# Kernel optimization log

Measured on AMD Instinct MI355X. Metric: run time of the kernel, lower is better.

Reference implementation:

```python
import jax, jax.numpy as jnp
import numpy as np

B, N, C = 32, 262144, 5
ALPHA = 50.0
EPS_LS = 0.2
BASE_W = [0.8, 2.0, 1.5, 1.5, 3.5]
# (cid, ref, sign): height_diff = sign*(pr_z[cid] - gt_z[ref]); violation = sigmoid(-10*diff)
# Enumerates all z_above / z_below pairs in the hierarchy dict.
PAIRS = [(1, 2, -1.0), (1, 3, -1.0), (1, 4, -1.0),
         (2, 1, 1.0), (2, 3, -1.0), (2, 4, -1.0),
         (3, 1, 1.0), (3, 2, 1.0), (3, 4, -1.0),
         (4, 1, 1.0), (4, 2, 1.0), (4, 3, 1.0)]


def setup_inputs() -> dict:
    key = jax.random.key(0)
    k1, k2, k3 = jax.random.split(key, 3)
    outputs = jax.random.normal(k1, (B, C, N), dtype=jnp.float32)
    labels = jax.random.randint(k2, (B, N), 0, C, dtype=jnp.int32)
    points = jax.random.normal(k3, (B, N, 3), dtype=jnp.float32)
    return {"outputs": outputs, "labels": labels, "points": points}


def _centroid(points, mask):
    # points: [B,N,3], mask: [B,N] bool -> ([B,3], [B] valid)
    valid = mask.any(axis=1)
    m = mask.astype(points.dtype)
    s = jnp.einsum('bn,bnd->bd', m, points)
    cnt = jnp.clip(m.sum(axis=1), 1.0)
    return s / cnt[:, None], valid


def _forward(outputs, points, labels):
    logits = jnp.transpose(outputs, (0, 2, 1))  # [B,N,C]
    b = labels.shape[0]
    preds = jnp.argmax(logits, axis=-1)  # [B,N]
    base = jnp.asarray(BASE_W, dtype=logits.dtype)
    weights = jnp.broadcast_to(base, (b, C))
    gt_c = {cid: _centroid(points, labels == cid) for cid in (1, 2, 3, 4)}
    pr_c = {cid: _centroid(points, preds == cid) for cid in (1, 2, 3, 4)}
    # hierarchy violation scatter into per-batch class weights
    for cid, ref, sign in PAIRS:
        pr_pos, pos_valid = pr_c[cid]
        gt_ref, ref_valid = gt_c[ref]
        valid = ref_valid & pos_valid
        diff = sign * (pr_pos[:, 2] - gt_ref[:, 2])
        add = jnp.where(valid, ALPHA * jax.nn.sigmoid(-diff * 10.0), 0.0)
        weights = weights.at[:, cid].add(add).at[:, ref].add(0.3 * add)
    # predicted bounding boxes of masked points (zeros included, as in torch)
    bounds = {}
    for cid in (2, 3):
        mp = points * (preds == cid)[:, :, None].astype(points.dtype)
        bounds[cid] = jnp.stack([mp.min(axis=1), mp.max(axis=1)], axis=1)  # [B,2,3]
    for cid in (2, 3):
        rb = bounds[3 if cid == 2 else 2]
        xc = (bounds[cid][:, :, 0] - rb[:, 0:1, 0]) / (rb[:, 1:2, 0] - rb[:, 0:1, 0] + 1e-7)
        yc = (bounds[cid][:, :, 1] - rb[:, 0:1, 1]) / (rb[:, 1:2, 1] - rb[:, 0:1, 1] + 1e-7)
        viol = ((xc < 0.1) | (xc > 0.9)) | ((yc < 0.1) | (yc > 0.9))
        weights = weights.at[:, cid].add(ALPHA * viol.astype(weights.dtype).mean(axis=1))
    weights = jnp.clip(weights, 0.1, 10.0)
    # inverse-sqrt class frequency weights
    dist = jnp.bincount(labels.reshape(-1), length=C).astype(logits.dtype)
    cw = 1.0 / (jnp.sqrt(dist) + 1e-7)
    cw = cw / cw.sum() * C
    w = weights.mean(axis=0) * cw  # [C]
    # weighted cross entropy with label_smoothing=0.2 (PyTorch semantics)
    logp = jax.nn.log_softmax(logits.reshape(-1, C), axis=-1)
    y = labels.reshape(-1)
    wt = w[y]
    wsum = wt.sum()
    nll = (wt * -jnp.take_along_axis(logp, y[:, None], axis=1)[:, 0]).sum() / wsum
    smooth = (-(logp * w[None, :]).sum(axis=-1)).sum() / wsum
    return (1.0 - EPS_LS) * nll + (EPS_LS / C) * smooth


def reference(outputs, labels, points):
    return _forward(outputs, points, labels)
```

## Files before the change

### kernel.cpp

```cpp
#include <hip/hip_runtime.h>
#include <math.h>

#define NPTS 262144
#define BATCH 32

__device__ __forceinline__ float wred_sum(float v) {
#pragma unroll
    for (int o = 32; o; o >>= 1) v += __shfl_down(v, o);
    return v;
}
__device__ __forceinline__ unsigned wred_usum(unsigned v) {
#pragma unroll
    for (int o = 32; o; o >>= 1) v += __shfl_down(v, o);
    return v;
}


__global__ __launch_bounds__(256) void bsl_main(
    const float* __restrict__ outputs, const int* __restrict__ labels,
    const float* __restrict__ points, float* __restrict__ pf,
    unsigned int* __restrict__ pi, int bpb, int iters,
    unsigned int* __restrict__ counter)
{
    const int blk = blockIdx.x;
    const int nblk = gridDim.x;
    const int b = blk / bpb;
    const int seg = blk % bpb;
    const int seg_start = seg * (iters * 1024);
    const int tid = threadIdx.x;

    if (blk == 0 && tid == 0) *counter = 0u;

    float S[5] = {0, 0, 0, 0, 0};
    float T[5] = {0, 0, 0, 0, 0};
    float lseacc = 0.f;
    float gtz[4] = {0, 0, 0, 0};
    float prz[4] = {0, 0, 0, 0};
    const float INF = __int_as_float(0x7f800000);
    float mn2x = INF, mx2x = -INF, mn2y = INF, mx2y = -INF;
    float mn3x = INF, mx3x = -INF, mn3y = INF, mx3y = -INF;
    unsigned bc[5] = {0, 0, 0, 0, 0}, prc[4] = {0, 0, 0, 0};

    const float* obase = outputs + (size_t)b * 5 * NPTS;
    const int*   lbase = labels + (size_t)b * NPTS;
    const float* pbase = points + (size_t)b * NPTS * 3;

    for (int it = 0; it < iters; ++it) {
        const int n = seg_start + it * 1024 + tid * 4;
        float4 L[5];
#pragma unroll
        for (int c = 0; c < 5; ++c)
            L[c] = *(const float4*)(obase + (size_t)c * NPTS + n);
        const int4 lab = *(const int4*)(lbase + n);
        const float4* pp = (const float4*)(pbase + (size_t)n * 3);
        const float4 p0 = pp[0], p1 = pp[1], p2 = pp[2];
        const float xs[4] = {p0.x, p0.w, p1.z, p2.y};
        const float ys[4] = {p0.y, p1.x, p1.w, p2.z};
        const float zs[4] = {p0.z, p1.y, p2.x, p2.w};
        const int   lb[4] = {lab.x, lab.y, lab.z, lab.w};
#pragma unroll
        for (int j = 0; j < 4; ++j) {
            float v[5];
#pragma unroll
            for (int c = 0; c < 5; ++c) v[c] = ((const float*)&L[c])[j];
            float best = v[0]; int pred = 0;
#pragma unroll
            for (int c = 1; c < 5; ++c)
                if (v[c] > best) { best = v[c]; pred = c; }
            float e = 0.f;
#pragma unroll
            for (int c = 0; c < 5; ++c) e += __expf(v[c] - best);
            const float lse = best + __logf(e);
            lseacc += lse;
            const int y = lb[j];
#pragma unroll
            for (int c = 0; c < 5; ++c) {
                S[c] += v[c];
                const bool is = (y == c);
                T[c] += is ? (lse - v[c]) : 0.f;
                bc[c] += is ? 1u : 0u;
            }
            const float z = zs[j];
#pragma unroll
            for (int k = 0; k < 4; ++k) {
                const bool gy = (y == k + 1), py = (pred == k + 1);
                gtz[k] += gy ? z : 0.f;
                prz[k] += py ? z : 0.f;
                prc[k] += py ? 1u : 0u;
            }
            const float x = xs[j], yv = ys[j];
            const float a2x = (pred == 2) ? x : 0.f;
            const float a2y = (pred == 2) ? yv : 0.f;
            const float a3x = (pred == 3) ? x : 0.f;
            const float a3y = (pred == 3) ? yv : 0.f;
            mn2x = fminf(mn2x, a2x); mx2x = fmaxf(mx2x, a2x);
            mn2y = fminf(mn2y, a2y); mx2y = fmaxf(mx2y, a2y);
            mn3x = fminf(mn3x, a3x); mx3x = fmaxf(mx3x, a3x);
            mn3y = fminf(mn3y, a3y); mx3y = fmaxf(mx3y, a3y);
        }
    }

    float fv[27] = {S[0], S[1], S[2], S[3], S[4],
                    T[0], T[1], T[2], T[3], T[4],
                    lseacc,
                    gtz[0], gtz[1], gtz[2], gtz[3],
                    prz[0], prz[1], prz[2], prz[3],
                    mn2x, mx2x, mn2y, mx2y, mn3x, mx3x, mn3y, mx3y};
    unsigned iv[9] = {bc[0], bc[1], bc[2], bc[3], bc[4],
                      prc[0], prc[1], prc[2], prc[3]};

    __shared__ float sf[4][27];
    __shared__ unsigned si[4][9];
    const int wid = tid >> 6, lane = tid & 63;
#pragma unroll
    for (int vdx = 0; vdx < 27; ++vdx) {
        float r;
        if (vdx < 19) r = wred_sum(fv[vdx]);
        else if (((vdx - 19) & 1) == 0) {
#pragma unroll
            for (int o = 32; o; o >>= 1) fv[vdx] = fminf(fv[vdx], __shfl_down(fv[vdx], o));
            r = fv[vdx];
        } else {
#pragma unroll
            for (int o = 32; o; o >>= 1) fv[vdx] = fmaxf(fv[vdx], __shfl_down(fv[vdx], o));
            r = fv[vdx];
        }
        if (lane == 0) sf[wid][vdx] = r;
    }
#pragma unroll
    for (int vdx = 0; vdx < 9; ++vdx) {
        unsigned r = wred_usum(iv[vdx]);
        if (lane == 0) si[wid][vdx] = r;
    }
    __syncthreads();
    if (tid == 0) {
#pragma unroll
        for (int vdx = 0; vdx < 27; ++vdx) {
            float r;
            if (vdx < 19) r = sf[0][vdx] + sf[1][vdx] + sf[2][vdx] + sf[3][vdx];
            else if (((vdx - 19) & 1) == 0)
                r = fminf(fminf(sf[0][vdx], sf[1][vdx]), fminf(sf[2][vdx], sf[3][vdx]));
            else
                r = fmaxf(fmaxf(sf[0][vdx], sf[1][vdx]), fmaxf(sf[2][vdx], sf[3][vdx]));
            pf[(size_t)vdx * nblk + blk] = r;
        }
#pragma unroll
        for (int vdx = 0; vdx < 9; ++vdx)
            pi[(size_t)vdx * nblk + blk] = si[0][vdx] + si[1][vdx] + si[2][vdx] + si[3][vdx];
    }
}

__global__ __launch_bounds__(256) void bsl_tail(
    const float* __restrict__ pf, const unsigned int* __restrict__ pi,
    int bpb, float* __restrict__ s2, unsigned int* __restrict__ counter,
    float* __restrict__ out)
{
    const int nblk = BATCH * bpb;
    const int t = blockIdx.x;
    const int tid = threadIdx.x;
    const int wid = tid >> 6, lane = tid & 63;
    __shared__ float red[4];
    __shared__ int isLast;
    __shared__ float sm[16 + 24 * BATCH];

    if (t < 16) {
        float s;
        if (t < 11) {
            const float4* p4 = (const float4*)(pf + (size_t)t * nblk);
            const float4 a = p4[tid], b = p4[tid + 256];
            s = ((a.x + a.y) + (a.z + a.w)) + ((b.x + b.y) + (b.z + b.w));
        } else {
            const uint4* p4 = (const uint4*)(pi + (size_t)(t - 11) * nblk);
            const uint4 a = p4[tid], b = p4[tid + 256];
            s = ((float)a.x + (float)a.y + (float)a.z + (float)a.w) +
                ((float)b.x + (float)b.y + (float)b.z + (float)b.w);
        }
        s = wred_sum(s);
        if (lane == 0) red[wid] = s;
        __syncthreads();
        if (tid == 0) s2[t] = red[0] + red[1] + red[2] + red[3];
    } else {
        const int b = tid >> 3;
        const int k = tid & 7;
        const int base = b * bpb;
        const int f = t - 16;
        float r;
        if (f < 8) {
            const float4* p4 = (const float4*)(pf + (size_t)(11 + f) * nblk + base);
            const float4 a = p4[k], c = p4[k + 8];
            r = ((a.x + a.y) + (a.z + a.w)) + ((c.x + c.y) + (c.z + c.w));
#pragma unroll
            for (int o = 4; o; o >>= 1) r += __shfl_xor(r, o);
        } else if (f < 16) {
            const int g = f - 8;
            const bool ismin = ((g & 1) == 0);
            const float4* p4 = (const float4*)(pf + (size_t)(19 + g) * nblk + base);
            const float4 a = p4[k], c = p4[k + 8];
            if (ismin) {
                r = fminf(fminf(fminf(a.x, a.y), fminf(a.z, a.w)),
                          fminf(fminf(c.x, c.y), fminf(c.z, c.w)));
#pragma unroll
                for (int o = 4; o; o >>= 1) r = fminf(r, __shfl_xor(r, o));
            } else {
                r = fmaxf(fmaxf(fmaxf(a.x, a.y), fmaxf(a.z, a.w)),
                          fmaxf(fmaxf(c.x, c.y), fmaxf(c.z, c.w)));
#pragma unroll
                for (int o = 4; o; o >>= 1) r = fmaxf(r, __shfl_xor(r, o));
            }
        } else {
            const int g = f - 16;
            const int row = (g < 4) ? (1 + g) : (5 + (g - 4));
            const uint4* p4 = (const uint4*)(pi + (size_t)row * nblk + base);
            const uint4 a = p4[k], c = p4[k + 8];
            r = ((float)a.x + (float)a.y + (float)a.z + (float)a.w) +
                ((float)c.x + (float)c.y + (float)c.z + (float)c.w);
#pragma unroll
            for (int o = 4; o; o >>= 1) r += __shfl_xor(r, o);
        }
        if (k == 0) s2[16 + b * 24 + ((f < 8) ? f : (f < 16) ? (8 + f - 8) : (16 + f - 16))] = r;
        __syncthreads();
    }

    if (tid == 0) {
        __threadfence();
        const unsigned old = atomicAdd(counter, 1u);
        isLast = (old == (unsigned)(gridDim.x - 1)) ? 1 : 0;
    }
    __syncthreads();
    if (!isLast) return;
    __threadfence();

    for (int i = tid; i < 16 + 24 * BATCH; i += 256) sm[i] = s2[i];
    __syncthreads();
    if (wid != 0) return;

    const float BASE_W[5] = {0.8f, 2.0f, 1.5f, 1.5f, 3.5f};
    const int pc[12]  = {1, 1, 1, 2, 2, 2, 3, 3, 3, 4, 4, 4};
    const int prf[12] = {2, 3, 4, 1, 3, 4, 1, 2, 4, 1, 2, 3};
    const float ps[12] = {-1.f, -1.f, -1.f, 1.f, -1.f, -1.f, 1.f, 1.f, -1.f, 1.f, 1.f, 1.f};

    float w[5] = {0, 0, 0, 0, 0};
    if (lane < BATCH) {
        const float* R = sm + 16 + lane * 24;
        for (int c = 0; c < 5; ++c) w[c] = BASE_W[c];
        float gtm[4], prm[4];
        bool gv[4], pv[4];
#pragma unroll
        for (int k = 0; k < 4; ++k) {
            const float c1 = R[16 + k];
            gv[k] = (c1 > 0.f);
            gtm[k] = R[k] / fmaxf(c1, 1.f);
            const float c2 = R[20 + k];
            pv[k] = (c2 > 0.f);
            prm[k] = R[4 + k] / fmaxf(c2, 1.f);
        }
#pragma unroll
        for (int p = 0; p < 12; ++p) {
            const int cid = pc[p], ref = prf[p];
            float add = 0.f;
            if (pv[cid - 1] && gv[ref - 1]) {
                const float diff = ps[p] * (prm[cid - 1] - gtm[ref - 1]);
                add = 50.f / (1.f + expf(10.f * diff));
            }
            w[cid] += add;
            w[ref] += 0.3f * add;
        }
        const float mn2x = R[8],  mx2x = R[9],  mn2y = R[10], mx2y = R[11];
        const float mn3x = R[12], mx3x = R[13], mn3y = R[14], mx3y = R[15];
        {
            const float dx = mx3x - mn3x + 1e-7f, dy = mx3y - mn3y + 1e-7f;
            const float xc0 = (mn2x - mn3x) / dx, xc1 = (mx2x - mn3x) / dx;
            const float yc0 = (mn2y - mn3y) / dy, yc1 = (mx2y - mn3y) / dy;
            const float v0 = (xc0 < 0.1f || xc0 > 0.9f || yc0 < 0.1f || yc0 > 0.9f) ? 1.f : 0.f;
            const float v1 = (xc1 < 0.1f || xc1 > 0.9f || yc1 < 0.1f || yc1 > 0.9f) ? 1.f : 0.f;
            w[2] += 50.f * 0.5f * (v0 + v1);
        }
        {
            const float dx = mx2x - mn2x + 1e-7f, dy = mx2y - mn2y + 1e-7f;
            const float xc0 = (mn3x - mn2x) / dx, xc1 = (mx3x - mn2x) / dx;
            const float yc0 = (mn3y - mn2y) / dy, yc1 = (mx3y - mn2y) / dy;
            const float v0 = (xc0 < 0.1f || xc0 > 0.9f || yc0 < 0.1f || yc0 > 0.9f) ? 1.f : 0.f;
            const float v1 = (xc1 < 0.1f || xc1 > 0.9f || yc1 < 0.1f || yc1 > 0.9f) ? 1.f : 0.f;
            w[3] += 50.f * 0.5f * (v0 + v1);
        }
#pragma unroll
        for (int c = 0; c < 5; ++c)
            w[c] = fminf(fmaxf(w[c], 0.1f), 10.f);
    }
    float wsumc[5];
#pragma unroll
    for (int c = 0; c < 5; ++c) wsumc[c] = wred_sum(w[c]);

    if (lane == 0) {
        float dist[5], cw[5], s = 0.f;
#pragma unroll
        for (int c = 0; c < 5; ++c) {
            dist[c] = sm[11 + c];
            cw[c] = 1.f / (sqrtf(dist[c]) + 1e-7f);
            s += cw[c];
        }
        float wf[5], wsum = 0.f, W = 0.f, nllnum = 0.f, Ssum = 0.f;
#pragma unroll
        for (int c = 0; c < 5; ++c) {
            cw[c] = cw[c] / s * 5.f;
            wf[c] = (wsumc[c] / 32.f) * cw[c];
            wsum += wf[c] * dist[c];
            W += wf[c];
            nllnum += wf[c] * sm[5 + c];
            Ssum += wf[c] * sm[c];
        }
        const float nll = nllnum / wsum;
        const float smooth = (W * sm[10] - Ssum) / wsum;
        out[0] = 0.8f * nll + 0.04f * smooth;
    }
}

extern "C" void kernel_launch(void* const* d_in, const int* in_sizes, int n_in,
                              void* d_out, int out_size, void* d_ws, size_t ws_size,
                              hipStream_t stream) {
    const float* outputs = (const float*)d_in[0];
    const int*   labels  = (const int*)d_in[1];
    const float* points  = (const float*)d_in[2];
    float* out = (float*)d_out;

    const size_t S2N = 16 + 24 * BATCH;
    const int bpb = 64;
    const int nblk = BATCH * bpb;
    const int iters = NPTS / (bpb * 1024);

    float* pf = (float*)d_ws;
    unsigned int* pi = (unsigned int*)(pf + (size_t)27 * nblk);
    float* s2 = (float*)(pi + (size_t)9 * nblk);
    unsigned int* counter = (unsigned int*)(s2 + S2N);

    bsl_main<<<nblk, 256, 0, stream>>>(outputs, labels, points, pf, pi, bpb, iters, counter);
    bsl_tail<<<40, 256, 0, stream>>>(pf, pi, bpb, s2, counter, out);
}
```

Before: 68.24 us.

## Fuse main and tail kernels using atomic counter handoff to last blocks

```diff
diff --git a/kernel.cpp b/kernel.cpp
--- a/kernel.cpp
+++ b/kernel.cpp
@@ -3,6 +3,11 @@
 
 #define NPTS 262144
 #define BATCH 32
+#define BPB 64
+#define NBLK (BATCH * BPB)
+#define NTAIL 40
+#define THRESH (NBLK - NTAIL)
+#define S2N (16 + 24 * BATCH)
 
 __device__ __forceinline__ float wred_sum(float v) {
 #pragma unroll
@@ -15,21 +20,30 @@
     return v;
 }
 
-
-__global__ __launch_bounds__(256) void bsl_main(
+__device__ __forceinline__ void ast(float* p, float v) {
+    __hip_atomic_store(p, v, __ATOMIC_RELAXED, __HIP_MEMORY_SCOPE_AGENT);
+}
+__device__ __forceinline__ void astu(unsigned* p, unsigned v) {
+    __hip_atomic_store(p, v, __ATOMIC_RELAXED, __HIP_MEMORY_SCOPE_AGENT);
+}
+__device__ __forceinline__ float ald(float* p) {
+    return __hip_atomic_load(p, __ATOMIC_RELAXED, __HIP_MEMORY_SCOPE_AGENT);
+}
+__device__ __forceinline__ unsigned aldu(unsigned* p) {
+    return __hip_atomic_load(p, __ATOMIC_RELAXED, __HIP_MEMORY_SCOPE_AGENT);
+}
+
+
+__global__ __launch_bounds__(256) void bsl_fused(
     const float* __restrict__ outputs, const int* __restrict__ labels,
-    const float* __restrict__ points, float* __restrict__ pf,
-    unsigned int* __restrict__ pi, int bpb, int iters,
-    unsigned int* __restrict__ counter)
+    const float* __restrict__ points, float* pf, unsigned* pi,
+    float* s2, unsigned* counters, float* out, int iters)
 {
     const int blk = blockIdx.x;
-    const int nblk = gridDim.x;
-    const int b = blk / bpb;
-    const int seg = blk % bpb;
+    const int b = blk / BPB;
+    const int seg = blk % BPB;
     const int seg_start = seg * (iters * 1024);
     const int tid = threadIdx.x;
-
-    if (blk == 0 && tid == 0) *counter = 0u;
 
     float S[5] = {0, 0, 0, 0, 0};
     float T[5] = {0, 0, 0, 0, 0};
@@ -142,95 +156,97 @@
                 r = fminf(fminf(sf[0][vdx], sf[1][vdx]), fminf(sf[2][vdx], sf[3][vdx]));
             else
                 r = fmaxf(fmaxf(sf[0][vdx], sf[1][vdx]), fmaxf(sf[2][vdx], sf[3][vdx]));
-            pf[(size_t)vdx * nblk + blk] = r;
+            ast(&pf[(size_t)vdx * NBLK + blk], r);
         }
 #pragma unroll
         for (int vdx = 0; vdx < 9; ++vdx)
-            pi[(size_t)vdx * nblk + blk] = si[0][vdx] + si[1][vdx] + si[2][vdx] + si[3][vdx];
-    }
-}
-
-__global__ __launch_bounds__(256) void bsl_tail(
-    const float* __restrict__ pf, const unsigned int* __restrict__ pi,
-    int bpb, float* __restrict__ s2, unsigned int* __restrict__ counter,
-    float* __restrict__ out)
-{
-    const int nblk = BATCH * bpb;
-    const int t = blockIdx.x;
-    const int tid = threadIdx.x;
-    const int wid = tid >> 6, lane = tid & 63;
+            astu(&pi[(size_t)vdx * NBLK + blk],
+                 si[0][vdx] + si[1][vdx] + si[2][vdx] + si[3][vdx]);
+    }
+
+    __shared__ int s_task;
+    if (tid == 0) {
+        const unsigned old = __hip_atomic_fetch_add(
+            &counters[0], 1u, __ATOMIC_RELEASE, __HIP_MEMORY_SCOPE_AGENT);
+        const int t = (int)old - THRESH;
+        if (t >= 0) {
+            while (__hip_atomic_load(&counters[0], __ATOMIC_ACQUIRE,
+                                     __HIP_MEMORY_SCOPE_AGENT) < (unsigned)NBLK)
+                __builtin_amdgcn_s_sleep(2);
+        }
+        s_task = t;
+    }
+    __syncthreads();
+    const int t = s_task;
+    if (t < 0) return;
+
     __shared__ float red[4];
-    __shared__ int isLast;
-    __shared__ float sm[16 + 24 * BATCH];
-
     if (t < 16) {
-        float s;
+        float s = 0.f;
         if (t < 11) {
-            const float4* p4 = (const float4*)(pf + (size_t)t * nblk);
-            const float4 a = p4[tid], b = p4[tid + 256];
-            s = ((a.x + a.y) + (a.z + a.w)) + ((b.x + b.y) + (b.z + b.w));
+            float* row = pf + (size_t)t * NBLK;
+#pragma unroll
+            for (int k = 0; k < 8; ++k) s += ald(row + tid + k * 256);
         } else {
-            const uint4* p4 = (const uint4*)(pi + (size_t)(t - 11) * nblk);
-            const uint4 a = p4[tid], b = p4[tid + 256];
-            s = ((float)a.x + (float)a.y + (float)a.z + (float)a.w) +
-                ((float)b.x + (float)b.y + (float)b.z + (float)b.w);
+            unsigned* row = pi + (size_t)(t - 11) * NBLK;
+#pragma unroll
+            for (int k = 0; k < 8; ++k) s += (float)aldu(row + tid + k * 256);
         }
         s = wred_sum(s);
         if (lane == 0) red[wid] = s;
         __syncthreads();
-        if (tid == 0) s2[t] = red[0] + red[1] + red[2] + red[3];
+        if (tid == 0) ast(&s2[t], red[0] + red[1] + red[2] + red[3]);
     } else {
-        const int b = tid >> 3;
-        const int k = tid & 7;
-        const int base = b * bpb;
         const int f = t - 16;
+        const int bb = tid >> 3, k = tid & 7;
+        const int base = bb * BPB;
         float r;
         if (f < 8) {
-            const float4* p4 = (const float4*)(pf + (size_t)(11 + f) * nblk + base);
-            const float4 a = p4[k], c = p4[k + 8];
-            r = ((a.x + a.y) + (a.z + a.w)) + ((c.x + c.y) + (c.z + c.w));
+            float* row = pf + (size_t)(11 + f) * NBLK + base;
+            r = 0.f;
+#pragma unroll
+            for (int j = 0; j < 8; ++j) r += ald(row + k * 8 + j);
 #pragma unroll
             for (int o = 4; o; o >>= 1) r += __shfl_xor(r, o);
         } else if (f < 16) {
             const int g = f - 8;
-            const bool ismin = ((g & 1) == 0);
-            const float4* p4 = (const float4*)(pf + (size_t)(19 + g) * nblk + base);
-            const float4 a = p4[k], c = p4[k + 8];
-            if (ismin) {
-                r = fminf(fminf(fminf(a.x, a.y), fminf(a.z, a.w)),
-                          fminf(fminf(c.x, c.y), fminf(c.z, c.w)));
+            float* row = pf + (size_t)(19 + g) * NBLK + base;
+            r = ald(row + k * 8);
+            if ((g & 1) == 0) {
+#pragma unroll
+                for (int j = 1; j < 8; ++j) r = fminf(r, ald(row + k * 8 + j));
 #pragma unroll
                 for (int o = 4; o; o >>= 1) r = fminf(r, __shfl_xor(r, o));
             } else {
-                r = fmaxf(fmaxf(fmaxf(a.x, a.y), fmaxf(a.z, a.w)),
-                          fmaxf(fmaxf(c.x, c.y), fmaxf(c.z, c.w)));
+#pragma unroll
+                for (int j = 1; j < 8; ++j) r = fmaxf(r, ald(row + k * 8 + j));
 #pragma unroll
                 for (int o = 4; o; o >>= 1) r = fmaxf(r, __shfl_xor(r, o));
             }
         } else {
             const int g = f - 16;
-            const int row = (g < 4) ? (1 + g) : (5 + (g - 4));
-            const uint4* p4 = (const uint4*)(pi + (size_t)row * nblk + base);
-            const uint4 a = p4[k], c = p4[k + 8];
-            r = ((float)a.x + (float)a.y + (float)a.z + (float)a.w) +
-                ((float)c.x + (float)c.y + (float)c.z + (float)c.w);
+            const int rowi = (g < 4) ? (1 + g) : (5 + (g - 4));
+            unsigned* row = pi + (size_t)rowi * NBLK + base;
+            r = 0.f;
+#pragma unroll
+            for (int j = 0; j < 8; ++j) r += (float)aldu(row + k * 8 + j);
 #pragma unroll
             for (int o = 4; o; o >>= 1) r += __shfl_xor(r, o);
         }
-        if (k == 0) s2[16 + b * 24 + ((f < 8) ? f : (f < 16) ? (8 + f - 8) : (16 + f - 16))] = r;
-        __syncthreads();
-    }
-
+        if (k == 0) ast(&s2[16 + bb * 24 + f], r);
+    }
+
+    __shared__ int s_last;
     if (tid == 0) {
-        __threadfence();
-        const unsigned old = atomicAdd(counter, 1u);
-        isLast = (old == (unsigned)(gridDim.x - 1)) ? 1 : 0;
+        const unsigned old2 = __hip_atomic_fetch_add(
+            &counters[1], 1u, __ATOMIC_ACQ_REL, __HIP_MEMORY_SCOPE_AGENT);
+        s_last = (old2 == NTAIL - 1) ? 1 : 0;
     }
     __syncthreads();
-    if (!isLast) return;
-    __threadfence();
-
-    for (int i = tid; i < 16 + 24 * BATCH; i += 256) sm[i] = s2[i];
+    if (!s_last) return;
+
+    __shared__ float sm[S2N];
+    for (int i = tid; i < S2N; i += 256) sm[i] = ald(&s2[i]);
     __syncthreads();
     if (wid != 0) return;
 
@@ -265,20 +281,20 @@
             w[cid] += add;
             w[ref] += 0.3f * add;
         }
-        const float mn2x = R[8],  mx2x = R[9],  mn2y = R[10], mx2y = R[11];
-        const float mn3x = R[12], mx3x = R[13], mn3y = R[14], mx3y = R[15];
+        const float mn2x_ = R[8],  mx2x_ = R[9],  mn2y_ = R[10], mx2y_ = R[11];
+        const float mn3x_ = R[12], mx3x_ = R[13], mn3y_ = R[14], mx3y_ = R[15];
         {
-            const float dx = mx3x - mn3x + 1e-7f, dy = mx3y - mn3y + 1e-7f;
-            const float xc0 = (mn2x - mn3x) / dx, xc1 = (mx2x - mn3x) / dx;
-            const float yc0 = (mn2y - mn3y) / dy, yc1 = (mx2y - mn3y) / dy;
+            const float dx = mx3x_ - mn3x_ + 1e-7f, dy = mx3y_ - mn3y_ + 1e-7f;
+            const float xc0 = (mn2x_ - mn3x_) / dx, xc1 = (mx2x_ - mn3x_) / dx;
+            const float yc0 = (mn2y_ - mn3y_) / dy, yc1 = (mx2y_ - mn3y_) / dy;
             const float v0 = (xc0 < 0.1f || xc0 > 0.9f || yc0 < 0.1f || yc0 > 0.9f) ? 1.f : 0.f;
             const float v1 = (xc1 < 0.1f || xc1 > 0.9f || yc1 < 0.1f || yc1 > 0.9f) ? 1.f : 0.f;
             w[2] += 50.f * 0.5f * (v0 + v1);
         }
         {
-            const float dx = mx2x - mn2x + 1e-7f, dy = mx2y - mn2y + 1e-7f;
-            const float xc0 = (mn3x - mn2x) / dx, xc1 = (mx3x - mn2x) / dx;
-            const float yc0 = (mn3y - mn2y) / dy, yc1 = (mx3y - mn2y) / dy;
+            const float dx = mx2x_ - mn2x_ + 1e-7f, dy = mx2y_ - mn2y_ + 1e-7f;
+            const float xc0 = (mn3x_ - mn2x_) / dx, xc1 = (mx3x_ - mn2x_) / dx;
+            const float yc0 = (mn3y_ - mn2y_) / dy, yc1 = (mx3y_ - mn2y_) / dy;
             const float v0 = (xc0 < 0.1f || xc0 > 0.9f || yc0 < 0.1f || yc0 > 0.9f) ? 1.f : 0.f;
             const float v1 = (xc1 < 0.1f || xc1 > 0.9f || yc1 < 0.1f || yc1 > 0.9f) ? 1.f : 0.f;
             w[3] += 50.f * 0.5f * (v0 + v1);
@@ -323,16 +339,14 @@
     const float* points  = (const float*)d_in[2];
     float* out = (float*)d_out;
 
-    const size_t S2N = 16 + 24 * BATCH;
-    const int bpb = 64;
-    const int nblk = BATCH * bpb;
-    const int iters = NPTS / (bpb * 1024);
-
-    float* pf = (float*)d_ws;
-    unsigned int* pi = (unsigned int*)(pf + (size_t)27 * nblk);
-    float* s2 = (float*)(pi + (size_t)9 * nblk);
-    unsigned int* counter = (unsigned int*)(s2 + S2N);
-
-    bsl_main<<<nblk, 256, 0, stream>>>(outputs, labels, points, pf, pi, bpb, iters, counter);
-    bsl_tail<<<40, 256, 0, stream>>>(pf, pi, bpb, s2, counter, out);
-}
+    unsigned* counters = (unsigned*)d_ws;
+    float* s2 = (float*)((char*)d_ws + 16);
+    float* pf = s2 + S2N;
+    unsigned* pi = (unsigned*)(pf + (size_t)27 * NBLK);
+
+    const int iters = NPTS / (BPB * 1024);
+
+    hipMemsetAsync(counters, 0, 8, stream);
+    bsl_fused<<<NBLK, 256, 0, stream>>>(outputs, labels, points,
+                                        pf, pi, s2, counters, out, iters);
+}
```

New measurement: 132.5 us. 94.2% more time.

## Replace per-block partial writes and multi-block tail with global atomics

Applied to the files above, without the earlier changes.

```diff
diff --git a/kernel.cpp b/kernel.cpp
--- a/kernel.cpp
+++ b/kernel.cpp
@@ -3,6 +3,10 @@
 
 #define NPTS 262144
 #define BATCH 32
+#define BPB 64
+#define NBLK (BATCH * BPB)
+#define NREP 8
+
 
 __device__ __forceinline__ float wred_sum(float v) {
 #pragma unroll
@@ -15,21 +19,26 @@
     return v;
 }
 
+__device__ __forceinline__ unsigned mapf(float f) {
+    unsigned u = __float_as_uint(f);
+    return (u & 0x80000000u) ? ~u : (u | 0x80000000u);
+}
+__device__ __forceinline__ float unmapf(unsigned m) {
+    return (m & 0x80000000u) ? __uint_as_float(m ^ 0x80000000u)
+                             : __uint_as_float(~m);
+}
 
 __global__ __launch_bounds__(256) void bsl_main(
     const float* __restrict__ outputs, const int* __restrict__ labels,
-    const float* __restrict__ points, float* __restrict__ pf,
-    unsigned int* __restrict__ pi, int bpb, int iters,
-    unsigned int* __restrict__ counter)
+    const float* __restrict__ points,
+    float* gsum, unsigned* gcnt, float* bsum, unsigned* bcnt,
+    unsigned* bmn, unsigned* bmx, int iters)
 {
     const int blk = blockIdx.x;
-    const int nblk = gridDim.x;
-    const int b = blk / bpb;
-    const int seg = blk % bpb;
+    const int b = blk / BPB;
+    const int seg = blk % BPB;
     const int seg_start = seg * (iters * 1024);
     const int tid = threadIdx.x;
-
-    if (blk == 0 && tid == 0) *counter = 0u;
 
     float S[5] = {0, 0, 0, 0, 0};
     float T[5] = {0, 0, 0, 0, 0};
@@ -133,106 +142,61 @@
         if (lane == 0) si[wid][vdx] = r;
     }
     __syncthreads();
-    if (tid == 0) {
-#pragma unroll
-        for (int vdx = 0; vdx < 27; ++vdx) {
-            float r;
-            if (vdx < 19) r = sf[0][vdx] + sf[1][vdx] + sf[2][vdx] + sf[3][vdx];
-            else if (((vdx - 19) & 1) == 0)
-                r = fminf(fminf(sf[0][vdx], sf[1][vdx]), fminf(sf[2][vdx], sf[3][vdx]));
-            else
-                r = fmaxf(fmaxf(sf[0][vdx], sf[1][vdx]), fmaxf(sf[2][vdx], sf[3][vdx]));
-            pf[(size_t)vdx * nblk + blk] = r;
-        }
-#pragma unroll
-        for (int vdx = 0; vdx < 9; ++vdx)
-            pi[(size_t)vdx * nblk + blk] = si[0][vdx] + si[1][vdx] + si[2][vdx] + si[3][vdx];
-    }
-}
-
-__global__ __launch_bounds__(256) void bsl_tail(
-    const float* __restrict__ pf, const unsigned int* __restrict__ pi,
-    int bpb, float* __restrict__ s2, unsigned int* __restrict__ counter,
+
+    const int rep = blk & (NREP - 1);
+    if (tid < 27) {
+        float r = sf[0][tid];
+        if (tid < 19) {
+            r += sf[1][tid] + sf[2][tid] + sf[3][tid];
+        } else if (((tid - 19) & 1) == 0) {
+            r = fminf(fminf(r, sf[1][tid]), fminf(sf[2][tid], sf[3][tid]));
+        } else {
+            r = fmaxf(fmaxf(r, sf[1][tid]), fmaxf(sf[2][tid], sf[3][tid]));
+        }
+        if (tid < 11) {
+            atomicAdd(&gsum[rep * 11 + tid], r);
+        } else if (tid < 19) {
+            atomicAdd(&bsum[b * 8 + (tid - 11)], r);
+        } else {
+            const int g = tid - 19;
+            const unsigned m = mapf(r);
+            if ((g & 1) == 0) atomicMin(&bmn[b * 4 + (g >> 1)], m);
+            else              atomicMax(&bmx[b * 4 + (g >> 1)], m);
+        }
+    } else if (tid >= 32 && tid < 41) {
+        const int v = tid - 32;
+        const unsigned r = si[0][v] + si[1][v] + si[2][v] + si[3][v];
+        if (v < 5) {
+            atomicAdd(&gcnt[rep * 5 + v], r);
+            if (v >= 1) atomicAdd(&bcnt[b * 8 + (v - 1)], r);
+        } else {
+            atomicAdd(&bcnt[b * 8 + 4 + (v - 5)], r);
+        }
+    }
+}
+
+__global__ __launch_bounds__(64) void bsl_final(
+    const float* __restrict__ gsum, const unsigned* __restrict__ gcnt,
+    const float* __restrict__ bsum, const unsigned* __restrict__ bcnt,
+    const unsigned* __restrict__ bmn, const unsigned* __restrict__ bmx,
     float* __restrict__ out)
 {
-    const int nblk = BATCH * bpb;
-    const int t = blockIdx.x;
-    const int tid = threadIdx.x;
-    const int wid = tid >> 6, lane = tid & 63;
-    __shared__ float red[4];
-    __shared__ int isLast;
-    __shared__ float sm[16 + 24 * BATCH];
-
-    if (t < 16) {
-        float s;
-        if (t < 11) {
-            const float4* p4 = (const float4*)(pf + (size_t)t * nblk);
-            const float4 a = p4[tid], b = p4[tid + 256];
-            s = ((a.x + a.y) + (a.z + a.w)) + ((b.x + b.y) + (b.z + b.w));
-        } else {
-            const uint4* p4 = (const uint4*)(pi + (size_t)(t - 11) * nblk);
-            const uint4 a = p4[tid], b = p4[tid + 256];
-            s = ((float)a.x + (float)a.y + (float)a.z + (float)a.w) +
-                ((float)b.x + (float)b.y + (float)b.z + (float)b.w);
-        }
-        s = wred_sum(s);
-        if (lane == 0) red[wid] = s;
-        __syncthreads();
-        if (tid == 0) s2[t] = red[0] + red[1] + red[2] + red[3];
-    } else {
-        const int b = tid >> 3;
-        const int k = tid & 7;
-        const int base = b * bpb;
-        const int f = t - 16;
-        float r;
-        if (f < 8) {
-            const float4* p4 = (const float4*)(pf + (size_t)(11 + f) * nblk + base);
-            const float4 a = p4[k], c = p4[k + 8];
-            r = ((a.x + a.y) + (a.z + a.w)) + ((c.x + c.y) + (c.z + c.w));
-#pragma unroll
-            for (int o = 4; o; o >>= 1) r += __shfl_xor(r, o);
-        } else if (f < 16) {
-            const int g = f - 8;
-            const bool ismin = ((g & 1) == 0);
-            const float4* p4 = (const float4*)(pf + (size_t)(19 + g) * nblk + base);
-            const float4 a = p4[k], c = p4[k + 8];
-            if (ismin) {
-                r = fminf(fminf(fminf(a.x, a.y), fminf(a.z, a.w)),
-                          fminf(fminf(c.x, c.y), fminf(c.z, c.w)));
-#pragma unroll
-                for (int o = 4; o; o >>= 1) r = fminf(r, __shfl_xor(r, o));
-            } else {
-                r = fmaxf(fmaxf(fmaxf(a.x, a.y), fmaxf(a.z, a.w)),
-                          fmaxf(fmaxf(c.x, c.y), fmaxf(c.z, c.w)));
-#pragma unroll
-                for (int o = 4; o; o >>= 1) r = fmaxf(r, __shfl_xor(r, o));
-            }
-        } else {
-            const int g = f - 16;
-            const int row = (g < 4) ? (1 + g) : (5 + (g - 4));
-            const uint4* p4 = (const uint4*)(pi + (size_t)row * nblk + base);
-            const uint4 a = p4[k], c = p4[k + 8];
-            r = ((float)a.x + (float)a.y + (float)a.z + (float)a.w) +
-                ((float)c.x + (float)c.y + (float)c.z + (float)c.w);
-#pragma unroll
-            for (int o = 4; o; o >>= 1) r += __shfl_xor(r, o);
-        }
-        if (k == 0) s2[16 + b * 24 + ((f < 8) ? f : (f < 16) ? (8 + f - 8) : (16 + f - 16))] = r;
-        __syncthreads();
-    }
-
-    if (tid == 0) {
-        __threadfence();
-        const unsigned old = atomicAdd(counter, 1u);
-        isLast = (old == (unsigned)(gridDim.x - 1)) ? 1 : 0;
-    }
-    __syncthreads();
-    if (!isLast) return;
-    __threadfence();
-
-    for (int i = tid; i < 16 + 24 * BATCH; i += 256) sm[i] = s2[i];
-    __syncthreads();
-    if (wid != 0) return;
+    const int lane = threadIdx.x;
+    __shared__ float smg[16];
+
+    if (lane < 16) {
+        float s = 0.f;
+        if (lane < 11) {
+#pragma unroll
+            for (int r = 0; r < NREP; ++r) s += gsum[r * 11 + lane];
+        } else {
+            unsigned u = 0;
+#pragma unroll
+            for (int r = 0; r < NREP; ++r) u += gcnt[r * 5 + (lane - 11)];
+            s = (float)u;
+        }
+        smg[lane] = s;
+    }
 
     const float BASE_W[5] = {0.8f, 2.0f, 1.5f, 1.5f, 3.5f};
     const int pc[12]  = {1, 1, 1, 2, 2, 2, 3, 3, 3, 4, 4, 4};
@@ -241,18 +205,17 @@
 
     float w[5] = {0, 0, 0, 0, 0};
     if (lane < BATCH) {
-        const float* R = sm + 16 + lane * 24;
         for (int c = 0; c < 5; ++c) w[c] = BASE_W[c];
         float gtm[4], prm[4];
         bool gv[4], pv[4];
 #pragma unroll
         for (int k = 0; k < 4; ++k) {
-            const float c1 = R[16 + k];
-            gv[k] = (c1 > 0.f);
-            gtm[k] = R[k] / fmaxf(c1, 1.f);
-            const float c2 = R[20 + k];
-            pv[k] = (c2 > 0.f);
-            prm[k] = R[4 + k] / fmaxf(c2, 1.f);
+            const unsigned c1 = bcnt[lane * 8 + k];
+            gv[k] = (c1 > 0u);
+            gtm[k] = bsum[lane * 8 + k] / fmaxf((float)c1, 1.f);
+            const unsigned c2 = bcnt[lane * 8 + 4 + k];
+            pv[k] = (c2 > 0u);
+            prm[k] = bsum[lane * 8 + 4 + k] / fmaxf((float)c2, 1.f);
         }
 #pragma unroll
         for (int p = 0; p < 12; ++p) {
@@ -265,8 +228,10 @@
             w[cid] += add;
             w[ref] += 0.3f * add;
         }
-        const float mn2x = R[8],  mx2x = R[9],  mn2y = R[10], mx2y = R[11];
-        const float mn3x = R[12], mx3x = R[13], mn3y = R[14], mx3y = R[15];
+        const float mn2x = unmapf(bmn[lane * 4 + 0]), mx2x = unmapf(bmx[lane * 4 + 0]);
+        const float mn2y = unmapf(bmn[lane * 4 + 1]), mx2y = unmapf(bmx[lane * 4 + 1]);
+        const float mn3x = unmapf(bmn[lane * 4 + 2]), mx3x = unmapf(bmx[lane * 4 + 2]);
+        const float mn3y = unmapf(bmn[lane * 4 + 3]), mx3y = unmapf(bmx[lane * 4 + 3]);
         {
             const float dx = mx3x - mn3x + 1e-7f, dy = mx3y - mn3y + 1e-7f;
             const float xc0 = (mn2x - mn3x) / dx, xc1 = (mx2x - mn3x) / dx;
@@ -291,11 +256,12 @@
 #pragma unroll
     for (int c = 0; c < 5; ++c) wsumc[c] = wred_sum(w[c]);
 
+    __syncthreads();
     if (lane == 0) {
         float dist[5], cw[5], s = 0.f;
 #pragma unroll
         for (int c = 0; c < 5; ++c) {
-            dist[c] = sm[11 + c];
+            dist[c] = smg[11 + c];
             cw[c] = 1.f / (sqrtf(dist[c]) + 1e-7f);
             s += cw[c];
         }
@@ -306,11 +272,11 @@
             wf[c] = (wsumc[c] / 32.f) * cw[c];
             wsum += wf[c] * dist[c];
             W += wf[c];
-            nllnum += wf[c] * sm[5 + c];
-            Ssum += wf[c] * sm[c];
+            nllnum += wf[c] * smg[5 + c];
+            Ssum += wf[c] * smg[c];
         }
         const float nll = nllnum / wsum;
-        const float smooth = (W * sm[10] - Ssum) / wsum;
+        const float smooth = (W * smg[10] - Ssum) / wsum;
         out[0] = 0.8f * nll + 0.04f * smooth;
     }
 }
@@ -323,16 +289,19 @@
     const float* points  = (const float*)d_in[2];
     float* out = (float*)d_out;
 
-    const size_t S2N = 16 + 24 * BATCH;
-    const int bpb = 64;
-    const int nblk = BATCH * bpb;
-    const int iters = NPTS / (bpb * 1024);
-
-    float* pf = (float*)d_ws;
-    unsigned int* pi = (unsigned int*)(pf + (size_t)27 * nblk);
-    float* s2 = (float*)(pi + (size_t)9 * nblk);
-    unsigned int* counter = (unsigned int*)(s2 + S2N);
-
-    bsl_main<<<nblk, 256, 0, stream>>>(outputs, labels, points, pf, pi, bpb, iters, counter);
-    bsl_tail<<<40, 256, 0, stream>>>(pf, pi, bpb, s2, counter, out);
-}
+    char* base = (char*)d_ws;
+    float*    gsum = (float*)(base + 0);
+    unsigned* gcnt = (unsigned*)(base + 352);
+    float*    bsum = (float*)(base + 512);
+    unsigned* bcnt = (unsigned*)(base + 1536);
+    unsigned* bmx  = (unsigned*)(base + 2560);
+    unsigned* bmn  = (unsigned*)(base + 3072);
+
+    const int iters = NPTS / (BPB * 1024);
+
+    hipMemsetAsync(base, 0, 3072, stream);
+    hipMemsetAsync(base + 3072, 0xFF, 512, stream);
+    bsl_main<<<NBLK, 256, 0, stream>>>(outputs, labels, points,
+                                       gsum, gcnt, bsum, bcnt, bmn, bmx, iters);
+    bsl_final<<<1, 64, 0, stream>>>(gsum, gcnt, bsum, bcnt, bmn, bmx, out);
+}
```

Result: slower. 71.89 us (+5.3%).
